# Performance work log

Hardware: AMD Instinct MI355X
Metric: run time of the kernel (lower is better)

The kernel has to match this reference:

```python
import jax, jax.numpy as jnp
import numpy as np

N_NODES = 50000
IN_DIM = 256
HID = 128
OUT_DIM = 64
N_LAYERS = 3
N_EDGES = 800000
BATCH = 4096
BN_EPS = 1e-5
LRELU_SLOPE = 0.01


def setup_inputs() -> dict:
    key = jax.random.key(0)
    ks = jax.random.split(key, 24)
    inp = {}
    inp["x"] = jax.random.normal(ks[0], (N_NODES, IN_DIM), jnp.float32)
    inp["edge_index"] = jax.random.randint(ks[1], (2, N_EDGES), 0, N_NODES, dtype=jnp.int32)
    inp["drug_pos_ids"] = jax.random.randint(ks[2], (BATCH,), 0, N_NODES, dtype=jnp.int32)
    inp["target_pos_ids"] = jax.random.randint(ks[3], (BATCH,), 0, N_NODES, dtype=jnp.int32)
    inp["drug_neg_ids"] = jax.random.randint(ks[4], (BATCH,), 0, N_NODES, dtype=jnp.int32)
    inp["target_neg_ids"] = jax.random.randint(ks[5], (BATCH,), 0, N_NODES, dtype=jnp.int32)
    inp["adjacency_matrix"] = jnp.zeros((1, 1), jnp.float32)  # dead arg in original forward
    # GCN layer params (xavier-normal-ish scale, zero bias as in __init__)
    for i in range(N_LAYERS):
        din = IN_DIM if i == 0 else HID
        inp[f"gcn_w{i}"] = jax.random.normal(ks[6 + i], (HID, din), jnp.float32) * np.float32(np.sqrt(2.0 / (din + HID)))
        inp[f"gcn_b{i}"] = jnp.zeros((HID,), jnp.float32)
    inp["bn_gamma"] = jnp.ones((HID,), jnp.float32)
    inp["bn_beta"] = jnp.zeros((HID,), jnp.float32)
    inp["W_D"] = jax.random.normal(ks[10], (HID, HID), jnp.float32) * np.float32(np.sqrt(2.0 / HID))
    inp["W_T"] = jax.random.normal(ks[11], (HID, HID), jnp.float32) * np.float32(np.sqrt(2.0 / HID))
    inp["q_D"] = jax.random.normal(ks[12], (HID,), jnp.float32)
    inp["q_T"] = jax.random.normal(ks[13], (HID,), jnp.float32)
    inp["out_w"] = jax.random.normal(ks[14], (OUT_DIM, HID), jnp.float32) * np.float32(np.sqrt(1.0 / HID))
    inp["out_b"] = jnp.zeros((OUT_DIM,), jnp.float32)
    return inp


def gcn_conv(x, w, b, src, dst, num_nodes):
    # PyG GCNConv: h = x @ W^T, then symmetric-normalized aggregation with self-loops
    h = x @ w.T                                           # [N, HID]
    deg = 1.0 + jax.ops.segment_sum(jnp.ones(src.shape[0], h.dtype), dst, num_segments=num_nodes)
    dinv = jax.lax.rsqrt(deg)                             # [N]
    norm = dinv[src] * dinv[dst]                          # [E]
    agg = jax.ops.segment_sum(h[src] * norm[:, None], dst, num_segments=num_nodes)
    agg = agg + h * (dinv * dinv)[:, None]                # self-loop contribution
    return agg + b


def batchnorm(x, gamma, beta):
    # training-mode BatchNorm1d math (batch statistics, biased var)
    mean = jnp.mean(x, axis=0)
    var = jnp.mean(jnp.square(x - mean), axis=0)
    return (x - mean) * jax.lax.rsqrt(var + BN_EPS) * gamma + beta


def attention_pooling(emb, W, q):
    # emb: [L, N, H]; softmax over the layer axis L
    h = jax.nn.leaky_relu(jnp.einsum('lnh,kh->lnk', emb, W), negative_slope=LRELU_SLOPE)
    e = jnp.einsum('lnk,k->ln', h, q)                     # [L, N]
    alpha = jax.nn.softmax(e, axis=0)
    return jnp.einsum('lnh,ln->nh', emb, alpha)           # [N, H]


def reference(x, edge_index, drug_pos_ids, target_pos_ids, drug_neg_ids, target_neg_ids,
              adjacency_matrix, gcn_w0, gcn_b0, gcn_w1, gcn_b1, gcn_w2, gcn_b2,
              bn_gamma, bn_beta, W_D, W_T, q_D, q_T, out_w, out_b):
    src, dst = edge_index[0], edge_index[1]
    num_nodes = x.shape[0]
    gcn_params = [(gcn_w0, gcn_b0), (gcn_w1, gcn_b1), (gcn_w2, gcn_b2)]
    layer_embs = []
    h = x
    for w, b in gcn_params:
        h = jax.nn.relu(gcn_conv(h, w, b, src, dst, num_nodes))
        h = batchnorm(h, bn_gamma, bn_beta)
        # dropout: identity (eval mode)
        layer_embs.append(h)
    emb = jnp.stack(layer_embs, axis=0)                   # [L, N, H]
    z_D = attention_pooling(emb, W_D, q_D) @ out_w.T + out_b
    z_T = attention_pooling(emb, W_T, q_T) @ out_w.T + out_b
    return (z_D[drug_pos_ids], z_T[target_pos_ids], z_D[drug_neg_ids], z_T[target_neg_ids])
```

## Files before the change

kernel.cpp:

```cpp
#include <hip/hip_runtime.h>
#include <hip/hip_fp16.h>
#include <cstdint>

#define N_NODES 50000
#define IN_DIM  256
#define HID     128
#define OUT_DIM 64
#define N_EDGES 800000
#define BATCH   4096
#define BN_EPS  1e-5f
#define SLOPE   0.01f

typedef unsigned short u16;
typedef __attribute__((ext_vector_type(8))) short bf16x8;
typedef __attribute__((ext_vector_type(4))) float f32x4;
typedef __attribute__((ext_vector_type(4))) unsigned u32x4;

__device__ __forceinline__ u16 f2bf(float f) {
    union { float f; unsigned u; } v; v.f = f;
    unsigned r = v.u + 0x7FFF + ((v.u >> 16) & 1);
    return (u16)(r >> 16);
}
__device__ __forceinline__ float bf2f(u16 b) {
    union { unsigned u; float f; } v; v.u = ((unsigned)b) << 16;
    return v.f;
}
__device__ __forceinline__ void splitbf(float v, u16* hi, u16* lo) {
    u16 h = f2bf(v);
    *hi = h;
    *lo = f2bf(v - bf2f(h));
}

__device__ __forceinline__ void swz_store(u16* __restrict__ buf, int K, int n, int k, float v) {
    int KC = K >> 7;
    int chunk = (n >> 6) * KC + (k >> 7);
    int base = chunk * 16384 + ((n >> 4) & 3) * 2048 + ((k >> 5) & 3) * 512
             + (((k >> 3) & 3) * 16 + (n & 15)) * 8 + (k & 7);
    u16 hi, lo;
    splitbf(v, &hi, &lo);
    buf[base] = hi;
    buf[base + 8192] = lo;
}

#define BNP_SPREAD 64
#define BNACC_PER_LAYER (BNP_SPREAD * 256)


#define PW0 (HID * IN_DIM)
#define PW1 (PW0 + HID * HID)
#define PW2 (PW1 + HID * HID)
#define PWD (PW2 + HID * HID)
#define PWT (PWD + HID * HID)
#define POW (PWT + OUT_DIM * HID)
#define PBN (POW + 3 * BNACC_PER_LAYER)
#define PBC (PBN + 256)

__global__ void prep(const float* __restrict__ w0, const float* __restrict__ w1,
                     const float* __restrict__ w2, const float* __restrict__ WD,
                     const float* __restrict__ WT, const float* __restrict__ out_w,
                     u16* __restrict__ w0swz, u16* __restrict__ w1swz, u16* __restrict__ w2swz,
                     u16* __restrict__ wDTswz,
                     float* __restrict__ wt, float* __restrict__ bnacc3,
                     int* __restrict__ bucketCnt) {
    int i = blockIdx.x * 256 + threadIdx.x;
    if (i < PW0) {
        swz_store(w0swz, IN_DIM, i >> 8, i & 255, w0[i]);
    } else if (i < PW1) {
        int j = i - PW0; swz_store(w1swz, HID, j >> 7, j & 127, w1[j]);
    } else if (i < PW2) {
        int j = i - PW1; swz_store(w2swz, HID, j >> 7, j & 127, w2[j]);
    } else if (i < PWD) {
        int j = i - PW2; swz_store(wDTswz, HID, j >> 7, j & 127, WD[j]);
    } else if (i < PWT) {
        int j = i - PWD; swz_store(wDTswz + 32768, HID, j >> 7, j & 127, WT[j]);
    } else if (i < POW) {
        int j = i - PWT;
        wt[j] = out_w[(j & 63) * HID + (j >> 6)];
    } else if (i < PBN) {
        bnacc3[i - POW] = 0.f;
    } else if (i < PBC) {
        bucketCnt[i - PBN] = 0;
    }
}


#define NBKT 196
#define PASSA_CHUNK 2048
#define NB_A ((N_EDGES + PASSA_CHUNK - 1) / PASSA_CHUNK)

__global__ void bucket_count(const int* __restrict__ dst, int* __restrict__ bucketCnt) {
    __shared__ int hist[NBKT];
    int t = threadIdx.x;
    if (t < NBKT) hist[t] = 0;
    __syncthreads();
    int b0 = blockIdx.x * PASSA_CHUNK;
    int b1 = min(b0 + PASSA_CHUNK, N_EDGES);
    for (int i = b0 + t; i < b1; i += 256)
        atomicAdd(&hist[dst[i] >> 8], 1);
    __syncthreads();
    if (t < NBKT && hist[t] > 0) atomicAdd(&bucketCnt[t], hist[t]);
}

__global__ void bucket_scan(const int* __restrict__ bucketCnt, int* __restrict__ bucketBase,
                            int* __restrict__ gcursor, int* __restrict__ rowstart) {
    __shared__ int s[256];
    int t = threadIdx.x;
    int v = (t < NBKT) ? bucketCnt[t] : 0;
    s[t] = v;
    __syncthreads();
#pragma unroll
    for (int off = 1; off < 256; off <<= 1) {
        int tmp = (t >= off) ? s[t - off] : 0;
        __syncthreads();
        s[t] += tmp;
        __syncthreads();
    }
    if (t < NBKT) { bucketBase[t] = s[t] - v; gcursor[t] = s[t] - v; }
    if (t == 0) { bucketBase[NBKT] = N_EDGES; rowstart[N_NODES] = N_EDGES; }
}

__global__ void bucket_scatter(const int* __restrict__ src, const int* __restrict__ dst,
                               int* __restrict__ gcursor, unsigned* __restrict__ pairs) {
    __shared__ int hist[NBKT], base[NBKT], hist2[NBKT];
    int t = threadIdx.x;
    if (t < NBKT) { hist[t] = 0; hist2[t] = 0; }
    __syncthreads();
    int b0 = blockIdx.x * PASSA_CHUNK;
    int b1 = min(b0 + PASSA_CHUNK, N_EDGES);
    for (int i = b0 + t; i < b1; i += 256)
        atomicAdd(&hist[dst[i] >> 8], 1);
    __syncthreads();
    if (t < NBKT && hist[t] > 0) base[t] = atomicAdd(&gcursor[t], hist[t]);
    __syncthreads();
    for (int i = b0 + t; i < b1; i += 256) {
        int d = dst[i];
        int b = d >> 8;
        int lp = atomicAdd(&hist2[b], 1);
        pairs[base[b] + lp] = ((unsigned)(d & 255) << 16) | (unsigned)src[i];
    }
}

__global__ void bucket_build(const unsigned* __restrict__ pairs, const int* __restrict__ bucketBase,
                             int* __restrict__ rowstart, float* __restrict__ dinv,
                             u16* __restrict__ csr) {
    __shared__ int cnt[256], s[256], lcur[256];
    int b = blockIdx.x, t = threadIdx.x;
    int pb0 = bucketBase[b], pb1 = bucketBase[b + 1];
    cnt[t] = 0;
    __syncthreads();
    for (int i = pb0 + t; i < pb1; i += 256)
        atomicAdd(&cnt[pairs[i] >> 16], 1);
    __syncthreads();
    int v = cnt[t];
    s[t] = v;
    __syncthreads();
#pragma unroll
    for (int off = 1; off < 256; off <<= 1) {
        int tmp = (t >= off) ? s[t - off] : 0;
        __syncthreads();
        s[t] += tmp;
        __syncthreads();
    }
    int node = (b << 8) + t;
    int start = pb0 + s[t] - v;
    if (node < N_NODES) {
        rowstart[node] = start;
        dinv[node] = rsqrtf(1.0f + (float)v);
    }
    lcur[t] = start;
    __syncthreads();
    for (int i = pb0 + t; i < pb1; i += 256) {
        unsigned pr = pairs[i];
        int pos = atomicAdd(&lcur[pr >> 16], 1);
        csr[pos] = (u16)(pr & 0xFFFFu);
    }
}


template<bool F16A, bool BNA>
__global__ __launch_bounds__(256) void gemm_tile(const void* __restrict__ Av,
                                                 const float* __restrict__ bnacc,
                                                 const float* __restrict__ gamma,
                                                 const float* __restrict__ beta,
                                                 const u16* __restrict__ Bswz,
                                                 const float* __restrict__ dinv,
                                                 u16* __restrict__ Cout,
                                                 int M, int K) {
    __shared__ u16 Bs[32768];
    __shared__ float bnss_s[2 * HID];
    __shared__ float red[256];
    const int tid  = threadIdx.x;
    const int wave = tid >> 6, lane = tid & 63;
    const int lr   = lane & 15, quad = lane >> 4;
    const int rowBase = blockIdx.x * 64;
    const int KC = K >> 7;

    if (BNA) {
        float accv = 0.f;
#pragma unroll 8
        for (int p = 0; p < BNP_SPREAD; ++p)
            accv += bnacc[p * 256 + tid];
        red[tid] = accv;
        __syncthreads();
        if (tid < HID) {
            float st = red[tid], sqt = red[HID + tid];
            float mean = st * (1.0f / N_NODES);
            float var  = fmaxf(sqt * (1.0f / N_NODES) - mean * mean, 0.f);
            float sc   = gamma[tid] * rsqrtf(var + BN_EPS);
            bnss_s[tid] = sc;
            bnss_s[HID + tid] = beta[tid] - mean * sc;
        }
        __syncthreads();
    }

    f32x4 acc[8];
#pragma unroll
    for (int c = 0; c < 8; ++c) acc[c] = (f32x4){0.f, 0.f, 0.f, 0.f};

    const int arow = rowBase + wave * 16 + lr;
    const bool rv = arow < M;

    for (int kc = 0; kc < KC; ++kc) {
        if (kc) __syncthreads();
        const uint4* s0 = (const uint4*)(Bswz + (size_t)kc * 16384);
        const uint4* s1 = (const uint4*)(Bswz + (size_t)(KC + kc) * 16384);
        uint4* B4 = (uint4*)Bs;
#pragma unroll
        for (int i = 0; i < 8; ++i)
            B4[i * 256 + tid] = s0[i * 256 + tid];
#pragma unroll
        for (int i = 0; i < 8; ++i)
            B4[2048 + i * 256 + tid] = s1[i * 256 + tid];
        __syncthreads();

#pragma unroll
        for (int kkidx = 0; kkidx < 4; ++kkidx) {
            const int kcol = kc * 128 + kkidx * 32 + quad * 8;
            float av[8];
            if (rv) {
                if (F16A) {
                    const u16* ap = (const u16*)Av + (size_t)arow * K + kcol;
                    uint4 v = *(const uint4*)ap;
                    float2 p0 = __half22float2(*(const __half2*)&v.x);
                    float2 p1 = __half22float2(*(const __half2*)&v.y);
                    float2 p2 = __half22float2(*(const __half2*)&v.z);
                    float2 p3 = __half22float2(*(const __half2*)&v.w);
                    av[0] = p0.x; av[1] = p0.y; av[2] = p1.x; av[3] = p1.y;
                    av[4] = p2.x; av[5] = p2.y; av[6] = p3.x; av[7] = p3.y;
                } else {
                    const float* ap = (const float*)Av + (size_t)arow * K + kcol;
                    float4 v0 = ((const float4*)ap)[0];
                    float4 v1 = ((const float4*)ap)[1];
                    av[0] = v0.x; av[1] = v0.y; av[2] = v0.z; av[3] = v0.w;
                    av[4] = v1.x; av[5] = v1.y; av[6] = v1.z; av[7] = v1.w;
                }
            } else {
#pragma unroll
                for (int j = 0; j < 8; ++j) av[j] = 0.f;
            }
            if (BNA) {
#pragma unroll
                for (int j = 0; j < 8; ++j) {
                    float sc = bnss_s[kcol + j];
                    float sh = bnss_s[HID + kcol + j];
                    av[j] = fmaf(av[j], sc, sh);
                }
            }
            bf16x8 ah, al;
#pragma unroll
            for (int j = 0; j < 8; ++j) {
                u16 hi, lo;
                splitbf(av[j], &hi, &lo);
                ((u16*)&ah)[j] = hi; ((u16*)&al)[j] = lo;
            }
#pragma unroll
            for (int c = 0; c < 8; ++c) {
                const int lb = (c >> 2) * 16384 + (c & 3) * 2048 + kkidx * 512 + lane * 8;
                bf16x8 bh = *(const bf16x8*)&Bs[lb];
                bf16x8 bl = *(const bf16x8*)&Bs[lb + 8192];
                acc[c] = __builtin_amdgcn_mfma_f32_16x16x32_bf16(al, bh, acc[c], 0, 0, 0);
                acc[c] = __builtin_amdgcn_mfma_f32_16x16x32_bf16(ah, bl, acc[c], 0, 0, 0);
                acc[c] = __builtin_amdgcn_mfma_f32_16x16x32_bf16(ah, bh, acc[c], 0, 0, 0);
            }
        }
    }

    const int rowb = rowBase + wave * 16 + quad * 4;
#pragma unroll
    for (int reg = 0; reg < 4; ++reg) {
        int row = rowb + reg;
        if (row < M) {
            float dn = dinv[row];
#pragma unroll
            for (int c = 0; c < 8; ++c) {
                __half hv = __float2half(acc[c][reg] * dn);
                u16* dst = Cout + (size_t)(c >> 1) * ((size_t)N_NODES * 32)
                         + (size_t)row * 32 + (c & 1) * 16 + lr;
                *dst = *(u16*)&hv;
            }
        }
    }
}


__global__ __launch_bounds__(256) void pool_gemm(const u16* __restrict__ emb0,
                                                 const u16* __restrict__ emb1,
                                                 const u16* __restrict__ emb2,
                                                 const float* __restrict__ bnss3,
                                                 const int* __restrict__ dpos, const int* __restrict__ dneg,
                                                 const int* __restrict__ tpos, const int* __restrict__ tneg,
                                                 const u16* __restrict__ wDTswz,
                                                 const float* __restrict__ q_D, const float* __restrict__ q_T,
                                                 float* __restrict__ e_D, float* __restrict__ e_T) {
    __shared__ u16 Bs[32768];
    const int head = blockIdx.y;
    const u16* Bswz = wDTswz + head * 32768;
    const float* q  = head ? q_T : q_D;
    float* eo = head ? e_T : e_D;
    const int* ia = head ? tpos : dpos;
    const int* ib = head ? tneg : dneg;

    const int tid  = threadIdx.x;
    const int wave = tid >> 6, lane = tid & 63;
    const int lr   = lane & 15, quad = lane >> 4;
    const int rowBase = blockIdx.x * 64;

    const int arow = rowBase + wave * 16 + lr;
    const int l0 = arow >> 13, j0 = arow & 8191;
    const int node0 = (j0 < BATCH) ? ia[j0] : ib[j0 - BATCH];
    const u16* embs[3] = {emb0, emb1, emb2};
    const u16* A0 = embs[l0] + (size_t)node0 * HID;
    const float* bn0 = bnss3 + l0 * 2 * HID;

    f32x4 acc[8];
#pragma unroll
    for (int c = 0; c < 8; ++c) acc[c] = (f32x4){0.f, 0.f, 0.f, 0.f};

    uint4* B4 = (uint4*)Bs;
    const uint4* srcB = (const uint4*)Bswz;
#pragma unroll
    for (int i = 0; i < 16; ++i)
        B4[i * 256 + tid] = srcB[i * 256 + tid];
    __syncthreads();

#pragma unroll
    for (int kkidx = 0; kkidx < 4; ++kkidx) {
        const int kcol = kkidx * 32 + quad * 8;
        float av[8];
        {
            uint4 v = *(const uint4*)(A0 + kcol);
            float2 p0 = __half22float2(*(const __half2*)&v.x);
            float2 p1 = __half22float2(*(const __half2*)&v.y);
            float2 p2 = __half22float2(*(const __half2*)&v.z);
            float2 p3 = __half22float2(*(const __half2*)&v.w);
            av[0] = p0.x; av[1] = p0.y; av[2] = p1.x; av[3] = p1.y;
            av[4] = p2.x; av[5] = p2.y; av[6] = p3.x; av[7] = p3.y;
        }
#pragma unroll
        for (int j = 0; j < 8; ++j)
            av[j] = fmaf(av[j], bn0[kcol + j], bn0[HID + kcol + j]);
        bf16x8 ah, al;
#pragma unroll
        for (int j = 0; j < 8; ++j) {
            u16 hi, lo;
            splitbf(av[j], &hi, &lo);
            ((u16*)&ah)[j] = hi; ((u16*)&al)[j] = lo;
        }
#pragma unroll
        for (int c = 0; c < 8; ++c) {
            const int lb = (c >> 2) * 16384 + (c & 3) * 2048 + kkidx * 512 + lane * 8;
            bf16x8 bh = *(const bf16x8*)&Bs[lb];
            bf16x8 bl = *(const bf16x8*)&Bs[lb + 8192];
            acc[c] = __builtin_amdgcn_mfma_f32_16x16x32_bf16(al, bh, acc[c], 0, 0, 0);
            acc[c] = __builtin_amdgcn_mfma_f32_16x16x32_bf16(ah, bl, acc[c], 0, 0, 0);
            acc[c] = __builtin_amdgcn_mfma_f32_16x16x32_bf16(ah, bh, acc[c], 0, 0, 0);
        }
    }

    float qv[8];
#pragma unroll
    for (int c = 0; c < 8; ++c) qv[c] = q[c * 16 + lr];
    const int rowb = rowBase + wave * 16 + quad * 4;
#pragma unroll
    for (int reg = 0; reg < 4; ++reg) {
        float p = 0.f;
#pragma unroll
        for (int c = 0; c < 8; ++c) {
            float v = acc[c][reg];
            v = (v > 0.f) ? v : SLOPE * v;
            p = fmaf(v, qv[c], p);
        }
        p += __shfl_xor(p, 1);
        p += __shfl_xor(p, 2);
        p += __shfl_xor(p, 4);
        p += __shfl_xor(p, 8);
        if (lr == 0) eo[rowb + reg] = p;
    }
}


#define AGG_NG ((N_NODES + 127) / 128)

__global__ __launch_bounds__(256) void agg_slice(const u16* __restrict__ hblk,
                                                 const float* __restrict__ dinv,
                                                 const int* __restrict__ rowstart,
                                                 const u16* __restrict__ csr,
                                                 const float* __restrict__ bias,
                                                 u16* __restrict__ out,
                                                 float* __restrict__ bnpart) {
    __shared__ float s_s[32], s_sq[32];
    const int tid  = threadIdx.x;
    const int wave = tid >> 6, lane = tid & 63;
    const int slot = lane >> 2;
    const int ql   = lane & 3;
    const int x = blockIdx.x & 7;
    const int slice = x >> 1, sub = x & 1;
    const int g = blockIdx.x >> 3;
    const u16* hs = hblk + (size_t)slice * ((size_t)N_NODES * 32);
    if (tid < 32) { s_s[tid] = 0.f; s_sq[tid] = 0.f; }
    __syncthreads();

    float bs[8], bq[8];
#pragma unroll
    for (int j = 0; j < 8; ++j) { bs[j] = 0.f; bq[j] = 0.f; }

    int n = ((g * 2 + sub) * 4 + wave) * 16 + slot;
    if (n < N_NODES) {
        int s = rowstart[n], e1 = rowstart[n + 1];
        float a[8];
#pragma unroll
        for (int j = 0; j < 8; ++j) a[j] = 0.f;

        int e = s;
        for (; e + 3 < e1; e += 4) {
            int c0 = csr[e], c1 = csr[e + 1], c2 = csr[e + 2], c3 = csr[e + 3];
            uint4 w0 = ((const uint4*)(hs + (size_t)c0 * 32))[ql];
            uint4 w1 = ((const uint4*)(hs + (size_t)c1 * 32))[ql];
            uint4 w2 = ((const uint4*)(hs + (size_t)c2 * 32))[ql];
            uint4 w3 = ((const uint4*)(hs + (size_t)c3 * 32))[ql];
            {
                float2 p0 = __half22float2(*(const __half2*)&w0.x);
                float2 p1 = __half22float2(*(const __half2*)&w0.y);
                float2 p2 = __half22float2(*(const __half2*)&w0.z);
                float2 p3 = __half22float2(*(const __half2*)&w0.w);
                a[0] += p0.x; a[1] += p0.y; a[2] += p1.x; a[3] += p1.y;
                a[4] += p2.x; a[5] += p2.y; a[6] += p3.x; a[7] += p3.y;
            }
            {
                float2 p0 = __half22float2(*(const __half2*)&w1.x);
                float2 p1 = __half22float2(*(const __half2*)&w1.y);
                float2 p2 = __half22float2(*(const __half2*)&w1.z);
                float2 p3 = __half22float2(*(const __half2*)&w1.w);
                a[0] += p0.x; a[1] += p0.y; a[2] += p1.x; a[3] += p1.y;
                a[4] += p2.x; a[5] += p2.y; a[6] += p3.x; a[7] += p3.y;
            }
            {
                float2 p0 = __half22float2(*(const __half2*)&w2.x);
                float2 p1 = __half22float2(*(const __half2*)&w2.y);
                float2 p2 = __half22float2(*(const __half2*)&w2.z);
                float2 p3 = __half22float2(*(const __half2*)&w2.w);
                a[0] += p0.x; a[1] += p0.y; a[2] += p1.x; a[3] += p1.y;
                a[4] += p2.x; a[5] += p2.y; a[6] += p3.x; a[7] += p3.y;
            }
            {
                float2 p0 = __half22float2(*(const __half2*)&w3.x);
                float2 p1 = __half22float2(*(const __half2*)&w3.y);
                float2 p2 = __half22float2(*(const __half2*)&w3.z);
                float2 p3 = __half22float2(*(const __half2*)&w3.w);
                a[0] += p0.x; a[1] += p0.y; a[2] += p1.x; a[3] += p1.y;
                a[4] += p2.x; a[5] += p2.y; a[6] += p3.x; a[7] += p3.y;
            }
        }
        for (; e < e1; ++e) {
            int c0 = csr[e];
            uint4 w0 = ((const uint4*)(hs + (size_t)c0 * 32))[ql];
            float2 p0 = __half22float2(*(const __half2*)&w0.x);
            float2 p1 = __half22float2(*(const __half2*)&w0.y);
            float2 p2 = __half22float2(*(const __half2*)&w0.z);
            float2 p3 = __half22float2(*(const __half2*)&w0.w);
            a[0] += p0.x; a[1] += p0.y; a[2] += p1.x; a[3] += p1.y;
            a[4] += p2.x; a[5] += p2.y; a[6] += p3.x; a[7] += p3.y;
        }

        float dn = dinv[n];
        uint4 hw = ((const uint4*)(hs + (size_t)n * 32))[ql];
        float2 h0 = __half22float2(*(const __half2*)&hw.x);
        float2 h1 = __half22float2(*(const __half2*)&hw.y);
        float2 h2 = __half22float2(*(const __half2*)&hw.z);
        float2 h3 = __half22float2(*(const __half2*)&hw.w);
        float hv[8] = {h0.x, h0.y, h1.x, h1.y, h2.x, h2.y, h3.x, h3.y};
        float4 bv0 = ((const float4*)(bias + slice * 32 + ql * 8))[0];
        float4 bv1 = ((const float4*)(bias + slice * 32 + ql * 8))[1];
        float bb[8] = {bv0.x, bv0.y, bv0.z, bv0.w, bv1.x, bv1.y, bv1.z, bv1.w};
        float o[8];
#pragma unroll
        for (int j = 0; j < 8; ++j) {
            o[j] = fmaxf(fmaf(dn, a[j] + hv[j], bb[j]), 0.f);
            bs[j] += o[j];
            bq[j] = fmaf(o[j], o[j], bq[j]);
        }
        __half2 q0 = __floats2half2_rn(o[0], o[1]);
        __half2 q1 = __floats2half2_rn(o[2], o[3]);
        __half2 q2 = __floats2half2_rn(o[4], o[5]);
        __half2 q3 = __floats2half2_rn(o[6], o[7]);
        u32x4 ov;
        ov.x = *(unsigned*)&q0; ov.y = *(unsigned*)&q1;
        ov.z = *(unsigned*)&q2; ov.w = *(unsigned*)&q3;
        __builtin_nontemporal_store(ov, (u32x4*)(out + (size_t)n * HID + slice * 32) + ql);
    }

#pragma unroll
    for (int j = 0; j < 8; ++j) {
        bs[j] += __shfl_xor(bs[j], 4);
        bs[j] += __shfl_xor(bs[j], 8);
        bs[j] += __shfl_xor(bs[j], 16);
        bs[j] += __shfl_xor(bs[j], 32);
        bq[j] += __shfl_xor(bq[j], 4);
        bq[j] += __shfl_xor(bq[j], 8);
        bq[j] += __shfl_xor(bq[j], 16);
        bq[j] += __shfl_xor(bq[j], 32);
    }
    if (slot == 0) {
#pragma unroll
        for (int j = 0; j < 8; ++j) {
            atomicAdd(&s_s[ql * 8 + j], bs[j]);
            atomicAdd(&s_sq[ql * 8 + j], bq[j]);
        }
    }
    __syncthreads();
    float* bp = bnpart + (size_t)(blockIdx.x & (BNP_SPREAD - 1)) * 256;
    if (tid < 32)      atomicAdd(&bp[slice * 32 + tid], s_s[tid]);
    else if (tid < 64) atomicAdd(&bp[128 + slice * 32 + (tid - 32)], s_sq[tid - 32]);
}


__global__ void bn_finalize3(const float* __restrict__ bnacc3,
                             const float* __restrict__ gamma, const float* __restrict__ beta,
                             float* __restrict__ bnss3) {
    int l = blockIdx.x;
    int f = threadIdx.x;
    const float* acc = bnacc3 + (size_t)l * BNACC_PER_LAYER;
    float st = 0.f, sqt = 0.f;
    for (int p = 0; p < BNP_SPREAD; ++p) {
        st  += acc[p * 256 + f];
        sqt += acc[p * 256 + HID + f];
    }
    float mean = st * (1.0f / N_NODES);
    float var  = fmaxf(sqt * (1.0f / N_NODES) - mean * mean, 0.f);
    float sc   = gamma[f] * rsqrtf(var + BN_EPS);
    bnss3[l * 2 * HID + f] = sc;
    bnss3[l * 2 * HID + HID + f] = beta[f] - mean * sc;
}


__global__ __launch_bounds__(256) void head_fused(const u16* __restrict__ emb0,
                                                  const u16* __restrict__ emb1,
                                                  const u16* __restrict__ emb2,
                                                  const float* __restrict__ bnss3,
                                                  const int* __restrict__ dpos, const int* __restrict__ dneg,
                                                  const int* __restrict__ tpos, const int* __restrict__ tneg,
                                                  const float* __restrict__ e_D, const float* __restrict__ e_T,
                                                  const float* __restrict__ B,
                                                  const float* __restrict__ bias,
                                                  float* __restrict__ out) {
    __shared__ float Pl[HID][64];
    __shared__ float Bs[32][OUT_DIM];
    const int y = blockIdx.y;
    const int head = y & 1, seg = y >> 1;
    const int* ia = head ? tpos : dpos;
    const int* ib = head ? tneg : dneg;
    const float* e = head ? e_T : e_D;
    const int tid = threadIdx.x;

    {
        int r = tid >> 2;
        int part = tid & 3;
        int p = seg * BATCH + blockIdx.x * 64 + r;
        int node = (p < BATCH) ? ia[p] : ib[p - BATCH];
        float l0 = e[p], l1 = e[2 * BATCH + p], l2 = e[4 * BATCH + p];
        float m = fmaxf(l0, fmaxf(l1, l2));
        float a0 = expf(l0 - m), a1 = expf(l1 - m), a2 = expf(l2 - m);
        float inv = 1.0f / (a0 + a1 + a2);
        a0 *= inv; a1 *= inv; a2 *= inv;
        const u16* r0 = emb0 + (size_t)node * HID + part * 32;
        const u16* r1 = emb1 + (size_t)node * HID + part * 32;
        const u16* r2 = emb2 + (size_t)node * HID + part * 32;
#pragma unroll
        for (int c = 0; c < 32; c += 8) {
            uint4 v0 = *(const uint4*)(r0 + c);
            uint4 v1 = *(const uint4*)(r1 + c);
            uint4 v2 = *(const uint4*)(r2 + c);
            int f = part * 32 + c;
            float e0v[8], e1v[8], e2v[8];
            {
                float2 p0 = __half22float2(*(const __half2*)&v0.x);
                float2 p1 = __half22float2(*(const __half2*)&v0.y);
                float2 p2 = __half22float2(*(const __half2*)&v0.z);
                float2 p3 = __half22float2(*(const __half2*)&v0.w);
                e0v[0] = p0.x; e0v[1] = p0.y; e0v[2] = p1.x; e0v[3] = p1.y;
                e0v[4] = p2.x; e0v[5] = p2.y; e0v[6] = p3.x; e0v[7] = p3.y;
            }
            {
                float2 p0 = __half22float2(*(const __half2*)&v1.x);
                float2 p1 = __half22float2(*(const __half2*)&v1.y);
                float2 p2 = __half22float2(*(const __half2*)&v1.z);
                float2 p3 = __half22float2(*(const __half2*)&v1.w);
                e1v[0] = p0.x; e1v[1] = p0.y; e1v[2] = p1.x; e1v[3] = p1.y;
                e1v[4] = p2.x; e1v[5] = p2.y; e1v[6] = p3.x; e1v[7] = p3.y;
            }
            {
                float2 p0 = __half22float2(*(const __half2*)&v2.x);
                float2 p1 = __half22float2(*(const __half2*)&v2.y);
                float2 p2 = __half22float2(*(const __half2*)&v2.z);
                float2 p3 = __half22float2(*(const __half2*)&v2.w);
                e2v[0] = p0.x; e2v[1] = p0.y; e2v[2] = p1.x; e2v[3] = p1.y;
                e2v[4] = p2.x; e2v[5] = p2.y; e2v[6] = p3.x; e2v[7] = p3.y;
            }
#pragma unroll
            for (int u = 0; u < 8; ++u) {
                float b0 = fmaf(e0v[u], bnss3[f + u],           bnss3[HID + f + u]);
                float b1 = fmaf(e1v[u], bnss3[2 * HID + f + u], bnss3[3 * HID + f + u]);
                float b2 = fmaf(e2v[u], bnss3[4 * HID + f + u], bnss3[5 * HID + f + u]);
                Pl[f + u][r] = a0 * b0 + a1 * b1 + a2 * b2;
            }
        }
    }
    __syncthreads();

    const int tx = tid & 15, ty = tid >> 4;
    float acc[4][4];
#pragma unroll
    for (int i = 0; i < 4; ++i)
#pragma unroll
        for (int j = 0; j < 4; ++j) acc[i][j] = 0.f;

    for (int kk = 0; kk < HID; kk += 32) {
        if (kk) __syncthreads();
#pragma unroll
        for (int i = tid; i < (32 * OUT_DIM) / 4; i += 256) {
            int k  = i >> 4;
            int n4 = i & 15;
            *(float4*)&Bs[k][n4 * 4] = *(const float4*)(B + (size_t)(kk + k) * OUT_DIM + n4 * 4);
        }
        __syncthreads();
#pragma unroll 8
        for (int k = 0; k < 32; ++k) {
            float a[4], b[4];
#pragma unroll
            for (int i = 0; i < 4; ++i) a[i] = Pl[kk + k][ty * 4 + i];
#pragma unroll
            for (int j = 0; j < 4; ++j) b[j] = Bs[k][tx * 4 + j];
#pragma unroll
            for (int i = 0; i < 4; ++i)
#pragma unroll
                for (int j = 0; j < 4; ++j)
                    acc[i][j] = fmaf(a[i], b[j], acc[i][j]);
        }
    }

    float* C = out + (size_t)y * BATCH * OUT_DIM + (size_t)(blockIdx.x * 64) * OUT_DIM;
#pragma unroll
    for (int i = 0; i < 4; ++i) {
        int r = ty * 4 + i;
#pragma unroll
        for (int j = 0; j < 4; ++j)
            C[(size_t)r * OUT_DIM + tx * 4 + j] = acc[i][j] + bias[tx * 4 + j];
    }
}


extern "C" void kernel_launch(void* const* d_in, const int* in_sizes, int n_in,
                              void* d_out, int out_size, void* d_ws, size_t ws_size,
                              hipStream_t stream) {
    const float* x          = (const float*)d_in[0];
    const int*   ei         = (const int*)d_in[1];
    const int*   srcp       = ei;
    const int*   dstp       = ei + N_EDGES;
    const int*   drug_pos   = (const int*)d_in[2];
    const int*   target_pos = (const int*)d_in[3];
    const int*   drug_neg   = (const int*)d_in[4];
    const int*   target_neg = (const int*)d_in[5];
    const float* gcn_w[3]   = {(const float*)d_in[7], (const float*)d_in[9], (const float*)d_in[11]};
    const float* gcn_b[3]   = {(const float*)d_in[8], (const float*)d_in[10], (const float*)d_in[12]};
    const float* gamma      = (const float*)d_in[13];
    const float* beta       = (const float*)d_in[14];
    const float* W_D        = (const float*)d_in[15];
    const float* W_T        = (const float*)d_in[16];
    const float* q_D        = (const float*)d_in[17];
    const float* q_T        = (const float*)d_in[18];
    const float* out_w      = (const float*)d_in[19];
    const float* out_b      = (const float*)d_in[20];
    float*       out        = (float*)d_out;

    char* p = (char*)d_ws;
    auto alloc = [&](size_t bytes) -> char* {
        char* r = p;
        p += (bytes + 255) & ~(size_t)255;
        return r;
    };
    char*  reg1  = alloc(sizeof(float) * (size_t)N_NODES * HID);
    u16*   emb0  = (u16*)alloc(sizeof(u16) * (size_t)N_NODES * HID);
    u16*   emb1  = (u16*)alloc(sizeof(u16) * (size_t)N_NODES * HID);
    u16*   emb2  = (u16*)alloc(sizeof(u16) * (size_t)N_NODES * HID);
    float* ebuf  = (float*)alloc(sizeof(float) * (size_t)2 * 3 * 2 * BATCH);
    u16*   w0swz = (u16*)alloc(sizeof(u16) * 2 * HID * IN_DIM);
    u16*   w1swz = (u16*)alloc(sizeof(u16) * 2 * HID * HID);
    u16*   w2swz = (u16*)alloc(sizeof(u16) * 2 * HID * HID);
    u16*   wDTswz = (u16*)alloc(sizeof(u16) * 4 * HID * HID);
    float* wt    = (float*)alloc(sizeof(float) * OUT_DIM * HID);
    int*   rowstart = (int*)alloc(sizeof(int) * (N_NODES + 1));
    u16*   csr   = (u16*)alloc(sizeof(int) * N_EDGES);
    unsigned* pairs = (unsigned*)alloc(sizeof(unsigned) * N_EDGES);
    float* dinvp = (float*)alloc(sizeof(float) * N_NODES);
    int*   bucketCnt  = (int*)alloc(sizeof(int) * 256);
    int*   bucketBase = (int*)alloc(sizeof(int) * (NBKT + 1));
    int*   gcursor    = (int*)alloc(sizeof(int) * 256);
    float* bnacc3 = (float*)alloc(sizeof(float) * 3 * BNACC_PER_LAYER);
    float* bnss3  = (float*)alloc(sizeof(float) * 3 * 2 * HID);
    if ((size_t)(p - (char*)d_ws) > ws_size) return;

    u16*   hbuf = (u16*)reg1;
    float* e_D  = ebuf;
    float* e_T  = ebuf + 3 * 2 * BATCH;
    u16*   embp[3] = {emb0, emb1, emb2};
    const u16* wswz[3] = {w0swz, w1swz, w2swz};

    prep<<<(PBC + 255) / 256, 256, 0, stream>>>(
        gcn_w[0], gcn_w[1], gcn_w[2], W_D, W_T, out_w,
        w0swz, w1swz, w2swz, wDTswz, wt, bnacc3, bucketCnt);

    bucket_count<<<NB_A, 256, 0, stream>>>(dstp, bucketCnt);
    bucket_scan<<<1, 256, 0, stream>>>(bucketCnt, bucketBase, gcursor, rowstart);
    bucket_scatter<<<NB_A, 256, 0, stream>>>(srcp, dstp, gcursor, pairs);
    bucket_build<<<NBKT, 256, 0, stream>>>(pairs, bucketBase, rowstart, dinvp, csr);

    const int GB = (N_NODES + 63) / 64;
    for (int l = 0; l < 3; ++l) {
        int din = (l == 0) ? IN_DIM : HID;
        if (l == 0)
            gemm_tile<false, false><<<GB, 256, 0, stream>>>(
                x, nullptr, nullptr, nullptr, wswz[l], dinvp, hbuf, N_NODES, din);
        else
            gemm_tile<true, true><<<GB, 256, 0, stream>>>(
                embp[l - 1], bnacc3 + (size_t)(l - 1) * BNACC_PER_LAYER, gamma, beta,
                wswz[l], dinvp, hbuf, N_NODES, din);
        agg_slice<<<AGG_NG * 8, 256, 0, stream>>>(hbuf, dinvp, rowstart, csr, gcn_b[l],
                                                  embp[l], bnacc3 + (size_t)l * BNACC_PER_LAYER);
    }

    bn_finalize3<<<3, HID, 0, stream>>>(bnacc3, gamma, beta, bnss3);

    const int RG = 3 * 2 * BATCH;
    pool_gemm<<<dim3(RG / 64, 2), 256, 0, stream>>>(
        emb0, emb1, emb2, bnss3, drug_pos, drug_neg, target_pos, target_neg,
        wDTswz, q_D, q_T, e_D, e_T);

    head_fused<<<dim3(BATCH / 64, 4), 256, 0, stream>>>(
        emb0, emb1, emb2, bnss3, drug_pos, drug_neg, target_pos, target_neg,
        e_D, e_T, wt, out_b, out);
}
```

Baseline: 353.5 us.

## Fold BatchNorm into GCN weights and use fp16 MFMA for hidden layers

```diff
diff --git a/kernel.cpp b/kernel.cpp
--- a/kernel.cpp
+++ b/kernel.cpp
@@ -13,6 +13,7 @@
 
 typedef unsigned short u16;
 typedef __attribute__((ext_vector_type(8))) short bf16x8;
+typedef __attribute__((ext_vector_type(8))) _Float16 f16x8;
 typedef __attribute__((ext_vector_type(4))) float f32x4;
 typedef __attribute__((ext_vector_type(4))) unsigned u32x4;
 
@@ -31,46 +32,49 @@
     *lo = f2bf(v - bf2f(h));
 }
 
-__device__ __forceinline__ void swz_store(u16* __restrict__ buf, int K, int n, int k, float v) {
+__device__ __forceinline__ void swz_base(int K, int n, int k, int* base) {
     int KC = K >> 7;
     int chunk = (n >> 6) * KC + (k >> 7);
-    int base = chunk * 16384 + ((n >> 4) & 3) * 2048 + ((k >> 5) & 3) * 512
-             + (((k >> 3) & 3) * 16 + (n & 15)) * 8 + (k & 7);
+    *base = chunk * 16384 + ((n >> 4) & 3) * 2048 + ((k >> 5) & 3) * 512
+          + (((k >> 3) & 3) * 16 + (n & 15)) * 8 + (k & 7);
+}
+__device__ __forceinline__ void swz_store(u16* __restrict__ buf, int K, int n, int k, float v) {
+    int base; swz_base(K, n, k, &base);
     u16 hi, lo;
     splitbf(v, &hi, &lo);
     buf[base] = hi;
     buf[base + 8192] = lo;
 }
+__device__ __forceinline__ void swz_store_f16(u16* __restrict__ buf, int K, int n, int k, float v) {
+    int base; swz_base(K, n, k, &base);
+    __half h = __float2half(v);
+    __half l = __float2half(v - __half2float(h));
+    buf[base] = *(u16*)&h;
+    buf[base + 8192] = *(u16*)&l;
+}
 
 #define BNP_SPREAD 64
 #define BNACC_PER_LAYER (BNP_SPREAD * 256)
 
 
 #define PW0 (HID * IN_DIM)
-#define PW1 (PW0 + HID * HID)
-#define PW2 (PW1 + HID * HID)
-#define PWD (PW2 + HID * HID)
+#define PWD (PW0 + HID * HID)
 #define PWT (PWD + HID * HID)
 #define POW (PWT + OUT_DIM * HID)
 #define PBN (POW + 3 * BNACC_PER_LAYER)
 #define PBC (PBN + 256)
 
-__global__ void prep(const float* __restrict__ w0, const float* __restrict__ w1,
-                     const float* __restrict__ w2, const float* __restrict__ WD,
-                     const float* __restrict__ WT, const float* __restrict__ out_w,
-                     u16* __restrict__ w0swz, u16* __restrict__ w1swz, u16* __restrict__ w2swz,
-                     u16* __restrict__ wDTswz,
+__global__ void prep(const float* __restrict__ w0,
+                     const float* __restrict__ WD, const float* __restrict__ WT,
+                     const float* __restrict__ out_w,
+                     u16* __restrict__ w0swz, u16* __restrict__ wDTswz,
                      float* __restrict__ wt, float* __restrict__ bnacc3,
                      int* __restrict__ bucketCnt) {
     int i = blockIdx.x * 256 + threadIdx.x;
     if (i < PW0) {
-        swz_store(w0swz, IN_DIM, i >> 8, i & 255, w0[i]);
-    } else if (i < PW1) {
-        int j = i - PW0; swz_store(w1swz, HID, j >> 7, j & 127, w1[j]);
-    } else if (i < PW2) {
-        int j = i - PW1; swz_store(w2swz, HID, j >> 7, j & 127, w2[j]);
+        swz_store_f16(w0swz, IN_DIM, i >> 8, i & 255, w0[i]);
     } else if (i < PWD) {
-        int j = i - PW2; swz_store(wDTswz, HID, j >> 7, j & 127, WD[j]);
+        int j = i - PW0; swz_store(wDTswz, HID, j >> 7, j & 127, WD[j]);
     } else if (i < PWT) {
         int j = i - PWD; swz_store(wDTswz + 32768, HID, j >> 7, j & 127, WT[j]);
     } else if (i < POW) {
@@ -84,6 +88,46 @@
 }
 
 
+__global__ __launch_bounds__(256) void scaleB(const float* __restrict__ W,
+                                              const float* __restrict__ bnacc,
+                                              const float* __restrict__ gamma,
+                                              const float* __restrict__ beta,
+                                              u16* __restrict__ Bswz,
+                                              float* __restrict__ cbias) {
+    __shared__ float red[256];
+    __shared__ float sc[HID], sh[HID];
+    int tid = threadIdx.x;
+    float accv = 0.f;
+#pragma unroll 8
+    for (int p = 0; p < BNP_SPREAD; ++p)
+        accv += bnacc[p * 256 + tid];
+    red[tid] = accv;
+    __syncthreads();
+    if (tid < HID) {
+        float st = red[tid], sqt = red[HID + tid];
+        float mean = st * (1.0f / N_NODES);
+        float var  = fmaxf(sqt * (1.0f / N_NODES) - mean * mean, 0.f);
+        float s    = gamma[tid] * rsqrtf(var + BN_EPS);
+        sc[tid] = s;
+        sh[tid] = beta[tid] - mean * s;
+    }
+    __syncthreads();
+    int base = blockIdx.x * 2048 + tid * 8;
+#pragma unroll
+    for (int u = 0; u < 8; ++u) {
+        int j = base + u;
+        int n = j >> 7, k = j & 127;
+        swz_store_f16(Bswz, HID, n, k, sc[k] * W[j]);
+    }
+    if (blockIdx.x == 0 && tid < HID) {
+        float s = 0.f;
+        for (int k = 0; k < HID; ++k)
+            s = fmaf(sh[k], W[tid * HID + k], s);
+        cbias[tid] = s;
+    }
+}
+
+
 #define NBKT 196
 #define PASSA_CHUNK 2048
 #define NB_A ((N_EDGES + PASSA_CHUNK - 1) / PASSA_CHUNK)
@@ -177,41 +221,22 @@
 }
 
 
-template<bool F16A, bool BNA>
+template<int MODE>
 __global__ __launch_bounds__(256) void gemm_tile(const void* __restrict__ Av,
-                                                 const float* __restrict__ bnacc,
-                                                 const float* __restrict__ gamma,
-                                                 const float* __restrict__ beta,
                                                  const u16* __restrict__ Bswz,
                                                  const float* __restrict__ dinv,
+                                                 const float* __restrict__ cbias,
                                                  u16* __restrict__ Cout,
                                                  int M, int K) {
     __shared__ u16 Bs[32768];
-    __shared__ float bnss_s[2 * HID];
-    __shared__ float red[256];
+    __shared__ float cb_s[HID];
     const int tid  = threadIdx.x;
     const int wave = tid >> 6, lane = tid & 63;
     const int lr   = lane & 15, quad = lane >> 4;
     const int rowBase = blockIdx.x * 64;
     const int KC = K >> 7;
 
-    if (BNA) {
-        float accv = 0.f;
-#pragma unroll 8
-        for (int p = 0; p < BNP_SPREAD; ++p)
-            accv += bnacc[p * 256 + tid];
-        red[tid] = accv;
-        __syncthreads();
-        if (tid < HID) {
-            float st = red[tid], sqt = red[HID + tid];
-            float mean = st * (1.0f / N_NODES);
-            float var  = fmaxf(sqt * (1.0f / N_NODES) - mean * mean, 0.f);
-            float sc   = gamma[tid] * rsqrtf(var + BN_EPS);
-            bnss_s[tid] = sc;
-            bnss_s[HID + tid] = beta[tid] - mean * sc;
-        }
-        __syncthreads();
-    }
+    if (MODE == 1 && tid < HID) cb_s[tid] = cbias[tid];
 
     f32x4 acc[8];
 #pragma unroll
@@ -236,51 +261,48 @@
 #pragma unroll
         for (int kkidx = 0; kkidx < 4; ++kkidx) {
             const int kcol = kc * 128 + kkidx * 32 + quad * 8;
-            float av[8];
-            if (rv) {
-                if (F16A) {
-                    const u16* ap = (const u16*)Av + (size_t)arow * K + kcol;
-                    uint4 v = *(const uint4*)ap;
-                    float2 p0 = __half22float2(*(const __half2*)&v.x);
-                    float2 p1 = __half22float2(*(const __half2*)&v.y);
-                    float2 p2 = __half22float2(*(const __half2*)&v.z);
-                    float2 p3 = __half22float2(*(const __half2*)&v.w);
-                    av[0] = p0.x; av[1] = p0.y; av[2] = p1.x; av[3] = p1.y;
-                    av[4] = p2.x; av[5] = p2.y; av[6] = p3.x; av[7] = p3.y;
-                } else {
+            if (MODE == 1) {
+                f16x8 a;
+#pragma unroll
+                for (int j = 0; j < 8; ++j) ((_Float16*)&a)[j] = (_Float16)0.f;
+                if (rv)
+                    a = *(const f16x8*)((const u16*)Av + (size_t)arow * K + kcol);
+#pragma unroll
+                for (int c = 0; c < 8; ++c) {
+                    const int lb = (c >> 2) * 16384 + (c & 3) * 2048 + kkidx * 512 + lane * 8;
+                    f16x8 bh = *(const f16x8*)&Bs[lb];
+                    f16x8 bl = *(const f16x8*)&Bs[lb + 8192];
+                    acc[c] = __builtin_amdgcn_mfma_f32_16x16x32_f16(a, bh, acc[c], 0, 0, 0);
+                    acc[c] = __builtin_amdgcn_mfma_f32_16x16x32_f16(a, bl, acc[c], 0, 0, 0);
+                }
+            } else {
+                float av[8];
+                if (rv) {
                     const float* ap = (const float*)Av + (size_t)arow * K + kcol;
                     float4 v0 = ((const float4*)ap)[0];
                     float4 v1 = ((const float4*)ap)[1];
                     av[0] = v0.x; av[1] = v0.y; av[2] = v0.z; av[3] = v0.w;
                     av[4] = v1.x; av[5] = v1.y; av[6] = v1.z; av[7] = v1.w;
+                } else {
+#pragma unroll
+                    for (int j = 0; j < 8; ++j) av[j] = 0.f;
                 }
-            } else {
-#pragma unroll
-                for (int j = 0; j < 8; ++j) av[j] = 0.f;
-            }
-            if (BNA) {
+                f16x8 ah, al;
 #pragma unroll
                 for (int j = 0; j < 8; ++j) {
-                    float sc = bnss_s[kcol + j];
-                    float sh = bnss_s[HID + kcol + j];
-                    av[j] = fmaf(av[j], sc, sh);
+                    _Float16 h = (_Float16)av[j];
+                    ((_Float16*)&ah)[j] = h;
+                    ((_Float16*)&al)[j] = (_Float16)(av[j] - (float)h);
                 }
-            }
-            bf16x8 ah, al;
-#pragma unroll
-            for (int j = 0; j < 8; ++j) {
-                u16 hi, lo;
-                splitbf(av[j], &hi, &lo);
-                ((u16*)&ah)[j] = hi; ((u16*)&al)[j] = lo;
-            }
-#pragma unroll
-            for (int c = 0; c < 8; ++c) {
-                const int lb = (c >> 2) * 16384 + (c & 3) * 2048 + kkidx * 512 + lane * 8;
-                bf16x8 bh = *(const bf16x8*)&Bs[lb];
-                bf16x8 bl = *(const bf16x8*)&Bs[lb + 8192];
-                acc[c] = __builtin_amdgcn_mfma_f32_16x16x32_bf16(al, bh, acc[c], 0, 0, 0);
-                acc[c] = __builtin_amdgcn_mfma_f32_16x16x32_bf16(ah, bl, acc[c], 0, 0, 0);
-                acc[c] = __builtin_amdgcn_mfma_f32_16x16x32_bf16(ah, bh, acc[c], 0, 0, 0);
+#pragma unroll
+                for (int c = 0; c < 8; ++c) {
+                    const int lb = (c >> 2) * 16384 + (c & 3) * 2048 + kkidx * 512 + lane * 8;
+                    f16x8 bh = *(const f16x8*)&Bs[lb];
+                    f16x8 bl = *(const f16x8*)&Bs[lb + 8192];
+                    acc[c] = __builtin_amdgcn_mfma_f32_16x16x32_f16(al, bh, acc[c], 0, 0, 0);
+                    acc[c] = __builtin_amdgcn_mfma_f32_16x16x32_f16(ah, bl, acc[c], 0, 0, 0);
+                    acc[c] = __builtin_amdgcn_mfma_f32_16x16x32_f16(ah, bh, acc[c], 0, 0, 0);
+                }
             }
         }
     }
@@ -293,7 +315,9 @@
             float dn = dinv[row];
 #pragma unroll
             for (int c = 0; c < 8; ++c) {
-                __half hv = __float2half(acc[c][reg] * dn);
+                float v = acc[c][reg];
+                if (MODE == 1) v += cb_s[c * 16 + lr];
+                __half hv = __float2half(v * dn);
                 u16* dst = Cout + (size_t)(c >> 1) * ((size_t)N_NODES * 32)
                          + (size_t)row * 32 + (c & 1) * 16 + lr;
                 *dst = *(u16*)&hv;
@@ -708,6 +732,7 @@
     u16*   w2swz = (u16*)alloc(sizeof(u16) * 2 * HID * HID);
     u16*   wDTswz = (u16*)alloc(sizeof(u16) * 4 * HID * HID);
     float* wt    = (float*)alloc(sizeof(float) * OUT_DIM * HID);
+    float* cbias12 = (float*)alloc(sizeof(float) * 2 * HID);
     int*   rowstart = (int*)alloc(sizeof(int) * (N_NODES + 1));
     u16*   csr   = (u16*)alloc(sizeof(int) * N_EDGES);
     unsigned* pairs = (unsigned*)alloc(sizeof(unsigned) * N_EDGES);
@@ -723,11 +748,10 @@
     float* e_D  = ebuf;
     float* e_T  = ebuf + 3 * 2 * BATCH;
     u16*   embp[3] = {emb0, emb1, emb2};
-    const u16* wswz[3] = {w0swz, w1swz, w2swz};
+    u16*   wswz[3] = {w0swz, w1swz, w2swz};
 
     prep<<<(PBC + 255) / 256, 256, 0, stream>>>(
-        gcn_w[0], gcn_w[1], gcn_w[2], W_D, W_T, out_w,
-        w0swz, w1swz, w2swz, wDTswz, wt, bnacc3, bucketCnt);
+        gcn_w[0], W_D, W_T, out_w, w0swz, wDTswz, wt, bnacc3, bucketCnt);
 
     bucket_count<<<NB_A, 256, 0, stream>>>(dstp, bucketCnt);
     bucket_scan<<<1, 256, 0, stream>>>(bucketCnt, bucketBase, gcursor, rowstart);
@@ -737,13 +761,17 @@
     const int GB = (N_NODES + 63) / 64;
     for (int l = 0; l < 3; ++l) {
         int din = (l == 0) ? IN_DIM : HID;
-        if (l == 0)
-            gemm_tile<false, false><<<GB, 256, 0, stream>>>(
-                x, nullptr, nullptr, nullptr, wswz[l], dinvp, hbuf, N_NODES, din);
-        else
-            gemm_tile<true, true><<<GB, 256, 0, stream>>>(
-                embp[l - 1], bnacc3 + (size_t)(l - 1) * BNACC_PER_LAYER, gamma, beta,
-                wswz[l], dinvp, hbuf, N_NODES, din);
+        if (l == 0) {
+            gemm_tile<0><<<GB, 256, 0, stream>>>(
+                x, wswz[0], dinvp, nullptr, hbuf, N_NODES, din);
+        } else {
+            scaleB<<<8, 256, 0, stream>>>(
+                gcn_w[l], bnacc3 + (size_t)(l - 1) * BNACC_PER_LAYER, gamma, beta,
+                wswz[l], cbias12 + (size_t)(l - 1) * HID);
+            gemm_tile<1><<<GB, 256, 0, stream>>>(
+                embp[l - 1], wswz[l], dinvp, cbias12 + (size_t)(l - 1) * HID,
+                hbuf, N_NODES, din);
+        }
         agg_slice<<<AGG_NG * 8, 256, 0, stream>>>(hbuf, dinvp, rowstart, csr, gcn_b[l],
                                                   embp[l], bnacc3 + (size_t)l * BNACC_PER_LAYER);
     }
```

After: 359.7 us. No clear change (+1.7%).
